# Kernel optimization log

Measured on AMD Instinct MI355X. Metric: run time of the kernel, lower is better.

The kernel has to match this reference:

```python
import jax, jax.numpy as jnp
import numpy as np

S, B, D, H = 2048, 4, 1024, 16
HD = D // H  # 64
NEG = -1e9


def _rope_cache(seq_len, dim, base=10000.0):
    inv_freq = 1.0 / (base ** (jnp.arange(0, dim, 2, dtype=jnp.float32) / dim))
    pos = jnp.arange(seq_len, dtype=jnp.float32)
    freqs = jnp.einsum('i,j->ij', pos, inv_freq)          # [S, dim/2]
    emb = jnp.concatenate([freqs, freqs], axis=-1)         # [S, dim]
    return jnp.cos(emb)[None, None], jnp.sin(emb)[None, None]  # [1,1,S,dim]


def _apply_rotary(x, cos, sin):
    # rotated[..., ::2] = -x[..., 1::2]; rotated[..., 1::2] = x[..., ::2]
    x_even = x[..., ::2]
    x_odd = x[..., 1::2]
    rotated = jnp.stack([-x_odd, x_even], axis=-1).reshape(x.shape)
    return x * cos + rotated * sin


def setup_inputs() -> dict:
    key = jax.random.key(0)
    kx, kq, ko = jax.random.split(key, 3)
    x = jax.random.normal(kx, (S, B, D), dtype=jnp.float32)
    # additive causal mask, broadcastable over [B,H,S,S]
    causal = jnp.triu(jnp.full((S, S), NEG, dtype=jnp.float32), k=1)
    cos, sin = _rope_cache(S, HD)
    Wqkv = jax.random.normal(kq, (D, 3 * D), dtype=jnp.float32) * (D ** -0.5)
    Wout = jax.random.normal(ko, (D, D), dtype=jnp.float32) * (D ** -0.5)
    return {"x": x, "attn_mask": causal, "cos": cos, "sin": sin,
            "Wqkv": Wqkv, "Wout": Wout}


def reference(x, attn_mask, cos, sin, Wqkv, Wout):
    scale = 1.0 / jnp.sqrt(jnp.float32(HD))
    xb = jnp.swapaxes(x, 0, 1)                       # [B,S,D]
    qkv = jnp.einsum('bsd,de->bse', xb, Wqkv)        # [B,S,3D]
    q, k, v = jnp.split(qkv, 3, axis=-1)
    def heads(t):
        return t.reshape(B, S, H, HD).transpose(0, 2, 1, 3)  # [B,H,S,HD]
    q, k, v = heads(q), heads(k), heads(v)
    q = _apply_rotary(q, cos, sin)
    k = _apply_rotary(k, cos, sin)
    scores = jnp.einsum('bhsd,bhtd->bhst', q, k) * scale + attn_mask
    probs = jax.nn.softmax(scores, axis=-1)
    ctx = jnp.einsum('bhst,bhtd->bhsd', probs, v)
    ctx = ctx.transpose(0, 2, 1, 3).reshape(B, S, D)  # [B,S,D]
    out = jnp.einsum('bsd,de->bse', ctx, Wout)
    return jnp.swapaxes(out, 0, 1)                    # [S,B,D]
```

## Files before the change

### kernel.cpp

```cpp
#include <hip/hip_runtime.h>
#include <hip/hip_bf16.h>

#define S_LEN 2048
#define BATCH 4
#define DMODEL 1024
#define NHEAD 16
#define HDIM 64
#define E3 3072

typedef __bf16 bf16x8 __attribute__((ext_vector_type(8)));
typedef float f32x4 __attribute__((ext_vector_type(4)));

typedef const __attribute__((address_space(1))) void gvoid;
typedef __attribute__((address_space(3))) void lvoid;

__global__ void cast_f32_bf16(const float* __restrict__ src, __bf16* __restrict__ dst) {
    int i = (blockIdx.x * 256 + threadIdx.x) * 8;
    float4 a = *(const float4*)(src + i);
    float4 b = *(const float4*)(src + i + 4);
    bf16x8 v;
    v[0] = (__bf16)a.x; v[1] = (__bf16)a.y; v[2] = (__bf16)a.z; v[3] = (__bf16)a.w;
    v[4] = (__bf16)b.x; v[5] = (__bf16)b.y; v[6] = (__bf16)b.z; v[7] = (__bf16)b.w;
    *(bf16x8*)(dst + i) = v;
}

__global__ void transpose_f32_bf16(const float* __restrict__ src, __bf16* __restrict__ dst,
                                   int R, int C) {
    __shared__ float tile[32][33];
    int c0 = blockIdx.x * 32, r0 = blockIdx.y * 32;
    int tx = threadIdx.x, ty = threadIdx.y;
#pragma unroll
    for (int i = 0; i < 32; i += 8)
        tile[ty + i][tx] = src[(size_t)(r0 + ty + i) * C + c0 + tx];
    __syncthreads();
#pragma unroll
    for (int i = 0; i < 32; i += 8)
        dst[(size_t)(c0 + ty + i) * R + r0 + tx] = (__bf16)tile[tx][ty + i];
}

__global__ __launch_bounds__(256) void gemm_bt(
    const __bf16* __restrict__ A, const __bf16* __restrict__ BT, void* __restrict__ C,
    int K, int aSB, int aSS, int cSB, int cSS, int cF32) {
    __shared__ __bf16 lA[128 * 32];
    __shared__ __bf16 lB[128 * 32];

    const int tid = threadIdx.x;
    const int lane = tid & 63;
    const int quad = lane >> 4, l16 = lane & 15;
    const int wave = tid >> 6;
    const int wm = wave >> 1, wn = wave & 1;
    const int rm0 = blockIdx.y * 128;
    const int n0 = blockIdx.x * 128;
    const int bb = rm0 / S_LEN;
    const int s0 = rm0 % S_LEN;

    const int lrow = lane >> 2;
    const int lch = (lane & 3) * 8;
    const int row0 = wave * 32;
    const __bf16* gA0 = A + (size_t)bb * aSB + (size_t)(s0 + row0 + lrow) * aSS + lch;
    const __bf16* gA1 = A + (size_t)bb * aSB + (size_t)(s0 + row0 + 16 + lrow) * aSS + lch;
    const __bf16* gB0 = BT + (size_t)(n0 + row0 + lrow) * K + lch;
    const __bf16* gB1 = BT + (size_t)(n0 + row0 + 16 + lrow) * K + lch;
    __bf16* ldsA0 = &lA[row0 * 32];
    __bf16* ldsA1 = &lA[(row0 + 16) * 32];
    __bf16* ldsB0 = &lB[row0 * 32];
    __bf16* ldsB1 = &lB[(row0 + 16) * 32];

    f32x4 acc[4][4];
#pragma unroll
    for (int i = 0; i < 4; i++)
#pragma unroll
        for (int j = 0; j < 4; j++) acc[i][j] = (f32x4){0.f, 0.f, 0.f, 0.f};

    for (int k0 = 0; k0 < K; k0 += 32) {
        __builtin_amdgcn_global_load_lds((gvoid*)(gA0 + k0), (lvoid*)ldsA0, 16, 0, 0);
        __builtin_amdgcn_global_load_lds((gvoid*)(gA1 + k0), (lvoid*)ldsA1, 16, 0, 0);
        __builtin_amdgcn_global_load_lds((gvoid*)(gB0 + k0), (lvoid*)ldsB0, 16, 0, 0);
        __builtin_amdgcn_global_load_lds((gvoid*)(gB1 + k0), (lvoid*)ldsB1, 16, 0, 0);
        __syncthreads();

        bf16x8 aF[4], bF[4];
#pragma unroll
        for (int i = 0; i < 4; i++) {
            aF[i] = *(const bf16x8*)&lA[(wm * 64 + i * 16 + l16) * 32 + quad * 8];
            bF[i] = *(const bf16x8*)&lB[(wn * 64 + i * 16 + l16) * 32 + quad * 8];
        }
#pragma unroll
        for (int i = 0; i < 4; i++)
#pragma unroll
            for (int j = 0; j < 4; j++)
                acc[i][j] = __builtin_amdgcn_mfma_f32_16x16x32_bf16(aF[i], bF[j], acc[i][j], 0, 0, 0);
        __syncthreads();
    }

#pragma unroll
    for (int i = 0; i < 4; i++) {
        const int rl = wm * 64 + i * 16 + quad * 4;
#pragma unroll
        for (int r = 0; r < 4; r++) {
            const size_t rowOff = (size_t)bb * cSB + (size_t)(s0 + rl + r) * cSS + n0 + wn * 64 + l16;
            if (cF32) {
                float* cRow = (float*)C + rowOff;
#pragma unroll
                for (int j = 0; j < 4; j++) cRow[j * 16] = acc[i][j][r];
            } else {
                __bf16* cRow = (__bf16*)C + rowOff;
#pragma unroll
                for (int j = 0; j < 4; j++) cRow[j * 16] = (__bf16)acc[i][j][r];
            }
        }
    }
}

__global__ void rope_kernel(__bf16* __restrict__ qkv, const float* __restrict__ cosb,
                            const float* __restrict__ sinb) {
    int idx = blockIdx.x * 256 + threadIdx.x;
    int p2 = (idx & 31) * 2;
    int h = (idx >> 5) & 15;
    int part = (idx >> 9) & 1;
    int row = idx >> 10;
    int s = row & (S_LEN - 1);
    size_t base = (size_t)row * E3 + part * DMODEL + h * HDIM + p2;
    float x0 = (float)qkv[base];
    float x1 = (float)qkv[base + 1];
    float c0 = cosb[s * HDIM + p2];
    float c1 = cosb[s * HDIM + p2 + 1];
    float sn0 = sinb[s * HDIM + p2];
    float sn1 = sinb[s * HDIM + p2 + 1];
    qkv[base] = (__bf16)(x0 * c0 - x1 * sn0);
    qkv[base + 1] = (__bf16)(x1 * c1 + x0 * sn1);
}

#define VT_IDX(hd, t) ((hd) * 72 + ((hd) >> 4) * 8 + (t))

__global__ __launch_bounds__(256) void attn_kernel(const __bf16* __restrict__ qkv,
                                                   __bf16* __restrict__ ctx) {
    __shared__ __bf16 sK[64 * 72];
    __shared__ __bf16 sVT[64 * 72 + 32];
    __shared__ __bf16 sP[4 * 2 * 16 * 72];

    const int tid = threadIdx.x, lane = tid & 63, wave = tid >> 6;
    const int quad = lane >> 4, l16 = lane & 15;
    const int b = blockIdx.y >> 4, h = blockIdx.y & 15;
    const int pair = blockIdx.x;
    const int qtA = pair, qtB = 31 - pair;
    const int s0A = qtA * 64 + wave * 16;
    const int s0B = qtB * 64 + wave * 16;
    __bf16* PwA = &sP[wave * 2 * 16 * 72];
    __bf16* PwB = PwA + 16 * 72;

    const int srow = tid >> 2;
    const int c0 = (tid & 3) * 16;

    const float qscale = 0.125f * 1.44269504f;
    const __bf16* kBase = qkv + (size_t)(b * S_LEN + srow) * E3 + DMODEL + h * HDIM + c0;
    const __bf16* vBase = kBase + DMODEL;

    const __bf16* qbA = qkv + (size_t)(b * S_LEN + s0A) * E3 + h * HDIM + (size_t)l16 * E3;
    const __bf16* qbB = qkv + (size_t)(b * S_LEN + s0B) * E3 + h * HDIM + (size_t)l16 * E3;
    bf16x8 qfA0 = *(const bf16x8*)(qbA + quad * 8);
    bf16x8 qfA1 = *(const bf16x8*)(qbA + 32 + quad * 8);
    bf16x8 qfB0 = *(const bf16x8*)(qbB + quad * 8);
    bf16x8 qfB1 = *(const bf16x8*)(qbB + 32 + quad * 8);
#pragma unroll
    for (int i = 0; i < 8; i++) {
        qfA0[i] = (__bf16)((float)qfA0[i] * qscale);
        qfA1[i] = (__bf16)((float)qfA1[i] * qscale);
        qfB0[i] = (__bf16)((float)qfB0[i] * qscale);
        qfB1[i] = (__bf16)((float)qfB1[i] * qscale);
    }

    f32x4 oA[4], oB[4], lacA, lacB;
#pragma unroll
    for (int j = 0; j < 4; j++) {
        oA[j] = (f32x4){0.f, 0.f, 0.f, 0.f};
        oB[j] = (f32x4){0.f, 0.f, 0.f, 0.f};
    }
    lacA = (f32x4){0.f, 0.f, 0.f, 0.f};
    lacB = (f32x4){0.f, 0.f, 0.f, 0.f};

    bf16x8 ones;
#pragma unroll
    for (int i = 0; i < 8; i++) ones[i] = (__bf16)1.0f;

    const __bf16* kRow = kBase;
    const __bf16* vRow = vBase;
    bf16x8 k0 = *(const bf16x8*)kRow;
    bf16x8 k1 = *(const bf16x8*)(kRow + 8);
    bf16x8 v0 = *(const bf16x8*)vRow;
    bf16x8 v1 = *(const bf16x8*)(vRow + 8);

    const int nT = qtB + 1;
#pragma unroll 1
    for (int it = 0; it < nT; ++it) {
        const int t0 = it * 64;
        *(bf16x8*)&sK[srow * 72 + c0] = k0;
        *(bf16x8*)&sK[srow * 72 + c0 + 8] = k1;
#pragma unroll
        for (int i = 0; i < 8; i++) {
            sVT[VT_IDX(c0 + i, srow)] = v0[i];
            sVT[VT_IDX(c0 + 8 + i, srow)] = v1[i];
        }
        __syncthreads();

        if (it + 1 < nT) {
            kRow += (size_t)64 * E3;
            vRow += (size_t)64 * E3;
            k0 = *(const bf16x8*)kRow;
            k1 = *(const bf16x8*)(kRow + 8);
            v0 = *(const bf16x8*)vRow;
            v1 = *(const bf16x8*)(vRow + 8);
        }

        const bool aAct = (it <= qtA);

        f32x4 scA[4], scB[4];
#pragma unroll
        for (int j = 0; j < 4; j++) {
            bf16x8 kf0 = *(const bf16x8*)&sK[(j * 16 + l16) * 72 + quad * 8];
            bf16x8 kf1 = *(const bf16x8*)&sK[(j * 16 + l16) * 72 + 32 + quad * 8];
            f32x4 z = (f32x4){0.f, 0.f, 0.f, 0.f};
            z = __builtin_amdgcn_mfma_f32_16x16x32_bf16(qfB0, kf0, z, 0, 0, 0);
            scB[j] = __builtin_amdgcn_mfma_f32_16x16x32_bf16(qfB1, kf1, z, 0, 0, 0);
            if (aAct) {
                f32x4 za = (f32x4){0.f, 0.f, 0.f, 0.f};
                za = __builtin_amdgcn_mfma_f32_16x16x32_bf16(qfA0, kf0, za, 0, 0, 0);
                scA[j] = __builtin_amdgcn_mfma_f32_16x16x32_bf16(qfA1, kf1, za, 0, 0, 0);
            }
        }

        if (it == qtB) {
#pragma unroll
            for (int j = 0; j < 4; j++)
#pragma unroll
                for (int r = 0; r < 4; r++) {
                    int sq = s0B + quad * 4 + r, st = t0 + j * 16 + l16;
                    float val = (st > sq) ? -1e9f : scB[j][r];
                    PwB[(quad * 4 + r) * 72 + j * 16 + l16] = (__bf16)__builtin_exp2f(val);
                }
        } else {
#pragma unroll
            for (int j = 0; j < 4; j++)
#pragma unroll
                for (int r = 0; r < 4; r++)
                    PwB[(quad * 4 + r) * 72 + j * 16 + l16] = (__bf16)__builtin_exp2f(scB[j][r]);
        }
        if (aAct) {
            if (it == qtA) {
#pragma unroll
                for (int j = 0; j < 4; j++)
#pragma unroll
                    for (int r = 0; r < 4; r++) {
                        int sq = s0A + quad * 4 + r, st = t0 + j * 16 + l16;
                        float val = (st > sq) ? -1e9f : scA[j][r];
                        PwA[(quad * 4 + r) * 72 + j * 16 + l16] = (__bf16)__builtin_exp2f(val);
                    }
            } else {
#pragma unroll
                for (int j = 0; j < 4; j++)
#pragma unroll
                    for (int r = 0; r < 4; r++)
                        PwA[(quad * 4 + r) * 72 + j * 16 + l16] = (__bf16)__builtin_exp2f(scA[j][r]);
            }
        }

#pragma unroll
        for (int kt = 0; kt < 2; kt++) {
            bf16x8 pfB = *(const bf16x8*)&PwB[l16 * 72 + kt * 32 + quad * 8];
            bf16x8 pfA = pfB;
            if (aAct) pfA = *(const bf16x8*)&PwA[l16 * 72 + kt * 32 + quad * 8];
#pragma unroll
            for (int j = 0; j < 4; j++) {
                bf16x8 vf = *(const bf16x8*)&sVT[VT_IDX(j * 16 + l16, kt * 32 + quad * 8)];
                oB[j] = __builtin_amdgcn_mfma_f32_16x16x32_bf16(pfB, vf, oB[j], 0, 0, 0);
                if (aAct) oA[j] = __builtin_amdgcn_mfma_f32_16x16x32_bf16(pfA, vf, oA[j], 0, 0, 0);
            }
            lacB = __builtin_amdgcn_mfma_f32_16x16x32_bf16(pfB, ones, lacB, 0, 0, 0);
            if (aAct) lacA = __builtin_amdgcn_mfma_f32_16x16x32_bf16(pfA, ones, lacA, 0, 0, 0);
        }
        __syncthreads();
    }

#pragma unroll
    for (int r = 0; r < 4; r++) {
        float inv = 1.f / lacA[r];
        size_t crow = (size_t)(b * S_LEN + s0A + quad * 4 + r) * DMODEL + h * HDIM + l16;
#pragma unroll
        for (int j = 0; j < 4; j++) ctx[crow + j * 16] = (__bf16)(oA[j][r] * inv);
    }
#pragma unroll
    for (int r = 0; r < 4; r++) {
        float inv = 1.f / lacB[r];
        size_t crow = (size_t)(b * S_LEN + s0B + quad * 4 + r) * DMODEL + h * HDIM + l16;
#pragma unroll
        for (int j = 0; j < 4; j++) ctx[crow + j * 16] = (__bf16)(oB[j][r] * inv);
    }
}

extern "C" void kernel_launch(void* const* d_in, const int* in_sizes, int n_in,
                              void* d_out, int out_size, void* d_ws, size_t ws_size,
                              hipStream_t stream) {
    const float* x = (const float*)d_in[0];
    const float* cosb = (const float*)d_in[2];
    const float* sinb = (const float*)d_in[3];
    const float* Wqkv = (const float*)d_in[4];
    const float* Wout = (const float*)d_in[5];
    float* out = (float*)d_out;

    char* ws = (char*)d_ws;
    __bf16* qkv = (__bf16*)ws;
    __bf16* ctx = (__bf16*)(ws + 50331648);
    __bf16* WqkvT = (__bf16*)(ws + 50331648 + 16777216);
    __bf16* WoutT = (__bf16*)(ws + 50331648 + 16777216 + 6291456);
    __bf16* xb = ctx;

    cast_f32_bf16<<<(S_LEN * BATCH * DMODEL / 8) / 256, 256, 0, stream>>>(x, xb);
    transpose_f32_bf16<<<dim3(E3 / 32, DMODEL / 32), dim3(32, 8), 0, stream>>>(Wqkv, WqkvT, DMODEL, E3);
    transpose_f32_bf16<<<dim3(DMODEL / 32, DMODEL / 32), dim3(32, 8), 0, stream>>>(Wout, WoutT, DMODEL, DMODEL);

    gemm_bt<<<dim3(E3 / 128, (BATCH * S_LEN) / 128), 256, 0, stream>>>(
        xb, WqkvT, qkv, DMODEL,
        DMODEL, BATCH * DMODEL,
        S_LEN * E3, E3, 0);

    rope_kernel<<<(BATCH * S_LEN * 2 * DMODEL / 2) / 256, 256, 0, stream>>>(qkv, cosb, sinb);

    attn_kernel<<<dim3(16, BATCH * NHEAD), 256, 0, stream>>>(qkv, ctx);

    gemm_bt<<<dim3(DMODEL / 128, (BATCH * S_LEN) / 128), 256, 0, stream>>>(
        ctx, WoutT, out, DMODEL,
        S_LEN * DMODEL, DMODEL,
        DMODEL, BATCH * DMODEL, 1);
}
```

Measured before the change: 354.9 us.

## Pre-transpose V into a global buffer and add MFMA wave priority hints

Adds a kernel that transposes V per (batch, head) into a [HD, S] layout, stored temporarily in the output buffer. The attention kernel can then write V^T tiles into LDS with vector stores instead of the old scattered per-element writes. It also brackets the MFMA phases with s_setprio so waves doing matrix math get scheduling priority. The cost is an extra kernel launch and an extra read and write of V through global memory. Reusing d_out as scratch is safe only because the final GEMM overwrites it afterward.

```diff
diff --git a/kernel.cpp b/kernel.cpp
--- a/kernel.cpp
+++ b/kernel.cpp
@@ -36,6 +36,29 @@
 #pragma unroll
     for (int i = 0; i < 32; i += 8)
         dst[(size_t)(c0 + ty + i) * R + r0 + tx] = (__bf16)tile[tx][ty + i];
+}
+
+__global__ void transpose_v(const __bf16* __restrict__ qkv, __bf16* __restrict__ vt) {
+    __shared__ unsigned short tile[64][65];
+    int bh = blockIdx.y;
+    int s0 = blockIdx.x * 64;
+    int tx = threadIdx.x & 31, ty = threadIdx.x >> 5;
+    const __bf16* src = qkv + (size_t)(bh >> 4) * S_LEN * E3 + 2 * DMODEL + (bh & 15) * HDIM;
+#pragma unroll
+    for (int i = 0; i < 8; i++) {
+        ushort2 v = *(const ushort2*)(src + (size_t)(s0 + ty + i * 8) * E3 + 2 * tx);
+        tile[2 * tx][ty + i * 8] = v.x;
+        tile[2 * tx + 1][ty + i * 8] = v.y;
+    }
+    __syncthreads();
+    __bf16* dst = vt + (size_t)bh * HDIM * S_LEN + s0;
+#pragma unroll
+    for (int i = 0; i < 8; i++) {
+        ushort2 v;
+        v.x = tile[ty + i * 8][2 * tx];
+        v.y = tile[ty + i * 8][2 * tx + 1];
+        *(ushort2*)(dst + (size_t)(ty + i * 8) * S_LEN + 2 * tx) = v;
+    }
 }
 
 __global__ __launch_bounds__(256) void gemm_bt(
@@ -134,6 +157,7 @@
 #define VT_IDX(hd, t) ((hd) * 72 + ((hd) >> 4) * 8 + (t))
 
 __global__ __launch_bounds__(256) void attn_kernel(const __bf16* __restrict__ qkv,
+                                                   const __bf16* __restrict__ vt,
                                                    __bf16* __restrict__ ctx) {
     __shared__ __bf16 sK[64 * 72];
     __shared__ __bf16 sVT[64 * 72 + 32];
@@ -154,7 +178,7 @@
 
     const float qscale = 0.125f * 1.44269504f;
     const __bf16* kBase = qkv + (size_t)(b * S_LEN + srow) * E3 + DMODEL + h * HDIM + c0;
-    const __bf16* vBase = kBase + DMODEL;
+    const __bf16* vBase = vt + ((size_t)blockIdx.y * HDIM + srow) * S_LEN + c0;
 
     const __bf16* qbA = qkv + (size_t)(b * S_LEN + s0A) * E3 + h * HDIM + (size_t)l16 * E3;
     const __bf16* qbB = qkv + (size_t)(b * S_LEN + s0B) * E3 + h * HDIM + (size_t)l16 * E3;
@@ -196,16 +220,13 @@
         const int t0 = it * 64;
         *(bf16x8*)&sK[srow * 72 + c0] = k0;
         *(bf16x8*)&sK[srow * 72 + c0 + 8] = k1;
-#pragma unroll
-        for (int i = 0; i < 8; i++) {
-            sVT[VT_IDX(c0 + i, srow)] = v0[i];
-            sVT[VT_IDX(c0 + 8 + i, srow)] = v1[i];
-        }
+        *(bf16x8*)&sVT[VT_IDX(srow, c0)] = v0;
+        *(bf16x8*)&sVT[VT_IDX(srow, c0 + 8)] = v1;
         __syncthreads();
 
         if (it + 1 < nT) {
             kRow += (size_t)64 * E3;
-            vRow += (size_t)64 * E3;
+            vRow += 64;
             k0 = *(const bf16x8*)kRow;
             k1 = *(const bf16x8*)(kRow + 8);
             v0 = *(const bf16x8*)vRow;
@@ -215,6 +236,7 @@
         const bool aAct = (it <= qtA);
 
         f32x4 scA[4], scB[4];
+        __builtin_amdgcn_s_setprio(1);
 #pragma unroll
         for (int j = 0; j < 4; j++) {
             bf16x8 kf0 = *(const bf16x8*)&sK[(j * 16 + l16) * 72 + quad * 8];
@@ -228,6 +250,7 @@
                 scA[j] = __builtin_amdgcn_mfma_f32_16x16x32_bf16(qfA1, kf1, za, 0, 0, 0);
             }
         }
+        __builtin_amdgcn_s_setprio(0);
 
         if (it == qtB) {
 #pragma unroll
@@ -264,6 +287,7 @@
             }
         }
 
+        __builtin_amdgcn_s_setprio(1);
 #pragma unroll
         for (int kt = 0; kt < 2; kt++) {
             bf16x8 pfB = *(const bf16x8*)&PwB[l16 * 72 + kt * 32 + quad * 8];
@@ -278,6 +302,7 @@
             lacB = __builtin_amdgcn_mfma_f32_16x16x32_bf16(pfB, ones, lacB, 0, 0, 0);
             if (aAct) lacA = __builtin_amdgcn_mfma_f32_16x16x32_bf16(pfA, ones, lacA, 0, 0, 0);
         }
+        __builtin_amdgcn_s_setprio(0);
         __syncthreads();
     }
 
@@ -313,6 +338,7 @@
     __bf16* WqkvT = (__bf16*)(ws + 50331648 + 16777216);
     __bf16* WoutT = (__bf16*)(ws + 50331648 + 16777216 + 6291456);
     __bf16* xb = ctx;
+    __bf16* vtg = (__bf16*)d_out;
 
     cast_f32_bf16<<<(S_LEN * BATCH * DMODEL / 8) / 256, 256, 0, stream>>>(x, xb);
     transpose_f32_bf16<<<dim3(E3 / 32, DMODEL / 32), dim3(32, 8), 0, stream>>>(Wqkv, WqkvT, DMODEL, E3);
@@ -323,9 +349,11 @@
         DMODEL, BATCH * DMODEL,
         S_LEN * E3, E3, 0);
 
+    transpose_v<<<dim3(S_LEN / 64, BATCH * NHEAD), 256, 0, stream>>>(qkv, vtg);
+
     rope_kernel<<<(BATCH * S_LEN * 2 * DMODEL / 2) / 256, 256, 0, stream>>>(qkv, cosb, sinb);
 
-    attn_kernel<<<dim3(16, BATCH * NHEAD), 256, 0, stream>>>(qkv, ctx);
+    attn_kernel<<<dim3(16, BATCH * NHEAD), 256, 0, stream>>>(qkv, vtg, ctx);
 
     gemm_bt<<<dim3(DMODEL / 128, (BATCH * S_LEN) / 128), 256, 0, stream>>>(
         ctx, WoutT, out, DMODEL,
```

After: 349.3 us. Within noise of the previous version (-1.6%).
